# Optimization experiments

Measured on AMD Instinct MI355X. Metric: run time of the kernel, lower is better.

Reference implementation:

```python
import jax, jax.numpy as jnp
import numpy as np

C = 128      # in_channels == global_graph_width
T = 1024     # time_step_len
B = 32       # batch (scenes)
N = B * T    # total nodes
E = 16 * N   # edges


def setup_inputs() -> dict:
    key = jax.random.key(0)
    ks = jax.random.split(key, 10)
    s = 1.0 / np.sqrt(C)
    return {
        "x": jax.random.normal(ks[0], (N, C), dtype=jnp.float32),
        "edge_index": jax.random.randint(ks[1], (2, E), 0, N, dtype=jnp.int64),
        "valid_lens": jax.random.randint(ks[2], (B,), 1, T, dtype=jnp.int64),
        "time_step_len": T,
        "Wq": jax.random.uniform(ks[3], (C, C), jnp.float32, -s, s),
        "bq": jax.random.uniform(ks[4], (C,), jnp.float32, -s, s),
        "Wk": jax.random.uniform(ks[5], (C, C), jnp.float32, -s, s),
        "bk": jax.random.uniform(ks[6], (C,), jnp.float32, -s, s),
        "Wv": jax.random.uniform(ks[7], (C, C), jnp.float32, -s, s),
        "bv": jax.random.uniform(ks[8], (C,), jnp.float32, -s, s),
    }


def reference(x, edge_index, valid_lens, time_step_len, Wq, bq, Wk, bk, Wv, bv):
    # GlobalGraph.forward in eval mode (no random training mask), 1 layer.
    n_nodes, c = x.shape
    xr = x.reshape(-1, time_step_len, c)                    # [B, T, C]
    q = xr @ Wq.T + bq                                      # [B, T, C]
    k = xr @ Wk.T + bk
    v = xr @ Wv.T + bv
    scores = jnp.einsum("btc,bsc->bts", q, k)               # [B, T, T]
    # masked_softmax: each row (b, t) keeps first valid_lens[b] cols, rest -1e6
    col = jnp.arange(time_step_len)                         # [T]
    mask = col[None, None, :] < valid_lens[:, None, None]   # [B, 1, T]
    scores = jnp.where(mask, scores, -1000000.0)
    attn = jax.nn.softmax(scores, axis=-1)                  # [B, T, T]
    out = jnp.einsum("bts,bsc->btc", attn, v).reshape(-1, c)  # [N, C]
    # MessagePassing propagate, aggr='add', flow source_to_target:
    # out_i = sum_{(j->i) in edges} out_j
    src, dst = edge_index[0], edge_index[1]
    return jax.ops.segment_sum(out[src], dst, num_segments=n_nodes)
```

## Files before the change

### kernel.cpp

```cpp
#include <hip/hip_runtime.h>
#include <hip/hip_bf16.h>
#include <stdint.h>

typedef __attribute__((ext_vector_type(8))) short short8;
typedef __attribute__((ext_vector_type(4))) float f32x4;
typedef __attribute__((ext_vector_type(4))) uint32_t u32x4;

static constexpr int NN = 32768;
static constexpr int CC = 128;
static constexpr int TT = 1024;
static constexpr int BB = 32;
static constexpr int EE = 524288;
static constexpr int PAD = 96;
static constexpr unsigned POISON = 0xAAAAAAAAu;

__device__ __forceinline__ unsigned short f2b(float f) {
    uint32_t u = __builtin_bit_cast(uint32_t, f);
    u = (u + 0x7fffu + ((u >> 16) & 1u)) >> 16;
    return (unsigned short)u;
}
__device__ __forceinline__ float b2f(unsigned short u) {
    uint32_t v = ((uint32_t)u) << 16;
    return __builtin_bit_cast(float, v);
}
__device__ __forceinline__ uint32_t cvt_pk_bf16(float lo, float hi) {
    uint32_t r;
    asm("v_cvt_pk_bf16_f32 %0, %1, %2" : "=v"(r) : "v"(lo), "v"(hi));
    return r;
}
__device__ __forceinline__ short8 pack8(float4 f0, float4 f1) {
    u32x4 pk;
    pk[0] = cvt_pk_bf16(f0.x, f0.y); pk[1] = cvt_pk_bf16(f0.z, f0.w);
    pk[2] = cvt_pk_bf16(f1.x, f1.y); pk[3] = cvt_pk_bf16(f1.z, f1.w);
    return __builtin_bit_cast(short8, pk);
}

static constexpr int QP = 132;

__global__ __launch_bounds__(256) void k_qkv(
    const float* __restrict__ Wq, const float* __restrict__ Wk,
    const float* __restrict__ Wv,
    const float* __restrict__ x,
    const float* __restrict__ bq, const float* __restrict__ bk, const float* __restrict__ bv,
    unsigned short* __restrict__ Qb, unsigned short* __restrict__ Kb,
    unsigned short* __restrict__ VB)
{
    __shared__ unsigned short Wl[CC * CC];
    __shared__ unsigned short qsm[4][16 * QP];

    int wv   = threadIdx.x >> 6;
    int lane = threadIdx.x & 63;
    int l15  = lane & 15, quad = lane >> 4;
    int m0   = ((blockIdx.x << 2) + wv) << 4;
    unsigned short* myT = qsm[wv];

    short8 a[4];
    const float* xrow = x + (size_t)(m0 + l15) * CC + quad * 8;
#pragma unroll
    for (int kk = 0; kk < 4; kk++) {
        float4 f0 = *(const float4*)(xrow + kk * 32);
        float4 f1 = *(const float4*)(xrow + kk * 32 + 4);
        a[kk] = pack8(f0, f1);
    }

    int srow = threadIdx.x >> 1;
    int shalf = threadIdx.x & 1;

    const float* Ws[3] = {Wq, Wk, Wv};
    const float* Bs[3] = {bq, bk, bv};

    for (int m = 0; m < 3; m++) {
        __syncthreads();
        {
            const float* wsrc = Ws[m] + (size_t)srow * CC + shalf * 64;
#pragma unroll
            for (int j = 0; j < 8; j++) {
                float4 f0 = *(const float4*)(wsrc + j * 8);
                float4 f1 = *(const float4*)(wsrc + j * 8 + 4);
                short8 v = pack8(f0, f1);
                int byte = srow * 256 + shalf * 128 + j * 16;
                byte ^= (srow & 7) << 4;
                *(short8*)((char*)Wl + byte) = v;
            }
        }
        __syncthreads();

        const float* bias = Bs[m];
        if (m < 2) {
            for (int nt = 0; nt < 8; nt++) {
                int n0 = nt << 4;
                int n  = n0 + l15;
                f32x4 acc = {0.f, 0.f, 0.f, 0.f};
#pragma unroll
                for (int kk = 0; kk < 4; kk++) {
                    int byte = n * 256 + kk * 64 + quad * 16;
                    byte ^= (n & 7) << 4;
                    short8 bfrag = *(const short8*)((const char*)Wl + byte);
                    acc = __builtin_amdgcn_mfma_f32_16x16x32_bf16(a[kk], bfrag, acc, 0, 0, 0);
                }
                float bval = bias[n];
#pragma unroll
                for (int r = 0; r < 4; r++)
                    myT[(quad * 4 + r) * QP + n] = f2b(acc[r] + bval);
            }
            unsigned short* dstp = m ? Kb : Qb;
#pragma unroll
            for (int t = 0; t < 4; t++) {
                int g   = t * 64 + lane;
                int row = g >> 4;
                int gc  = (g & 15) * 8;
                short8 vvx = *(const short8*)&myT[row * QP + gc];
                *(short8*)&dstp[(size_t)(m0 + row) * CC + gc] = vvx;
            }
        } else {
            for (int nt = 0; nt < 8; nt++) {
                int n0 = nt << 4;
                int n  = n0 + l15;
                f32x4 acc = {0.f, 0.f, 0.f, 0.f};
#pragma unroll
                for (int kk = 0; kk < 4; kk++) {
                    int byte = n * 256 + kk * 64 + quad * 16;
                    byte ^= (n & 7) << 4;
                    short8 bfrag = *(const short8*)((const char*)Wl + byte);
                    acc = __builtin_amdgcn_mfma_f32_16x16x32_bf16(a[kk], bfrag, acc, 0, 0, 0);
                }
                float bval = bias[n];
                ushort4 pk;
                pk.x = f2b(acc[0] + bval); pk.y = f2b(acc[1] + bval);
                pk.z = f2b(acc[2] + bval); pk.w = f2b(acc[3] + bval);
                int b_  = m0 >> 10;
                int sb  = (m0 & (TT - 1)) >> 5;
                int sin = (m0 & 31) + quad * 4;
                *(ushort4*)&VB[((size_t)(b_ * 32 + sb) * CC + n) * 32 + sin] = pk;
            }
        }
    }
}

static constexpr int PITCH = 40;

__global__ __launch_bounds__(256, 2) void k_attn(
    const unsigned short* __restrict__ Qb, const unsigned short* __restrict__ Kb,
    const unsigned short* __restrict__ VB, const int* __restrict__ valid_lens,
    unsigned short* __restrict__ ao2,
    const int* __restrict__ ei, int* __restrict__ cnt, int* __restrict__ slot)
{
    __shared__ unsigned short Ksm[3][512 * 8];
    __shared__ unsigned short Vsm[3][512 * 8];
    __shared__ unsigned short pl[4][16 * PITCH];

    int bid  = blockIdx.x;
    int w    = threadIdx.x >> 6;
    int lane = threadIdx.x & 63;
    int l15  = lane & 15, quad = lane >> 4;
    int xcd = bid & 7, j = bid >> 3;
    int b   = xcd + ((j & 3) << 3);
    int qt  = j >> 2;
    int m0  = b * TT + qt * 64 + w * 16;
    int L   = valid_lens[b];
    int nsteps = (L + 31) >> 5;

    int g    = (w << 6) | lane;
    int ksr  = g >> 4,  ksc = ((g & 15) - ksr) & 15;
    int vch  = g >> 2,  vsg = ((g & 3) - (vch >> 1)) & 3;

    const unsigned short* Kbase = Kb + (size_t)b * TT * CC;
    const unsigned short* Vbase = VB + (size_t)b * 32 * CC * 32;

#define STAGE(bufi, s0g)                                                              \
    do {                                                                              \
        int _s0 = (s0g);                                                              \
        __builtin_amdgcn_global_load_lds(                                             \
            (const __attribute__((address_space(1))) uint32_t*)(Kbase + (size_t)(_s0 + ksr) * CC + ksc * 8), \
            (__attribute__((address_space(3))) uint32_t*)&Ksm[bufi][(size_t)(w << 6) * 8], 16, 0, 0);        \
        __builtin_amdgcn_global_load_lds(                                             \
            (const __attribute__((address_space(1))) uint32_t*)(Kbase + (size_t)(_s0 + 16 + ksr) * CC + ksc * 8), \
            (__attribute__((address_space(3))) uint32_t*)&Ksm[bufi][(size_t)((w << 6) + 256) * 8], 16, 0, 0);     \
        const unsigned short* _vt = Vbase + (size_t)(_s0 >> 5) * CC * 32;             \
        __builtin_amdgcn_global_load_lds(                                             \
            (const __attribute__((address_space(1))) uint32_t*)(_vt + vch * 32 + vsg * 8),                   \
            (__attribute__((address_space(3))) uint32_t*)&Vsm[bufi][(size_t)(w << 6) * 8], 16, 0, 0);        \
        __builtin_amdgcn_global_load_lds(                                             \
            (const __attribute__((address_space(1))) uint32_t*)(_vt + (vch + 64) * 32 + vsg * 8),            \
            (__attribute__((address_space(3))) uint32_t*)&Vsm[bufi][(size_t)((w << 6) + 256) * 8], 16, 0, 0);     \
    } while (0)

    short8 a[4];
    {
        const unsigned short* qrow = Qb + (size_t)(m0 + l15) * CC + quad * 8;
#pragma unroll
        for (int kk = 0; kk < 4; kk++) a[kk] = *(const short8*)(qrow + kk * 32);
    }

    f32x4 o[8];
#pragma unroll
    for (int ct = 0; ct < 8; ct++) o[ct] = (f32x4){0.f, 0.f, 0.f, 0.f};
    float l_[4] = {0.f, 0.f, 0.f, 0.f};

    unsigned short* myP = pl[w];

    STAGE(0, 0);
    if (nsteps > 1) STAGE(1, 32);

    for (int i = 0; i < nsteps; i++) {
        int s0 = i << 5;
        int bufi = i - (i / 3) * 3;
        int rem = nsteps - 1 - i;
        if (rem >= 1) asm volatile("s_waitcnt vmcnt(4)" ::: "memory");
        else          asm volatile("s_waitcnt vmcnt(0)" ::: "memory");
        __builtin_amdgcn_s_barrier();
        __builtin_amdgcn_sched_barrier(0);

        const unsigned short* Kc = Ksm[bufi];
        const unsigned short* Vc = Vsm[bufi];

        f32x4 S0 = {0.f,0.f,0.f,0.f}, S1 = {0.f,0.f,0.f,0.f};
        __builtin_amdgcn_s_setprio(1);
#pragma unroll
        for (int kk = 0; kk < 4; kk++) {
            int cidx = kk * 4 + quad;
            int t0 = (cidx + l15) & 15;
            short8 b0 = *(const short8*)&Kc[(size_t)(l15 * 16 + t0) * 8];
            short8 b1 = *(const short8*)&Kc[(size_t)(((16 | l15) * 16) + t0) * 8];
            S0 = __builtin_amdgcn_mfma_f32_16x16x32_bf16(a[kk], b0, S0, 0, 0, 0);
            S1 = __builtin_amdgcn_mfma_f32_16x16x32_bf16(a[kk], b1, S1, 0, 0, 0);
        }
        __builtin_amdgcn_s_setprio(0);

        bool ok0 = (s0 + l15) < L;
        bool ok1 = (s0 + 16 + l15) < L;
        float p0[4], p1[4];
#pragma unroll
        for (int r = 0; r < 4; r++) {
            p0[r] = ok0 ? __expf(S0[r]) : 0.f;
            p1[r] = ok1 ? __expf(S1[r]) : 0.f;
            l_[r] += p0[r] + p1[r];
        }
#pragma unroll
        for (int r = 0; r < 4; r++) {
            int row = quad * 4 + r;
            myP[row * PITCH + l15]      = f2b(p0[r]);
            myP[row * PITCH + 16 + l15] = f2b(p1[r]);
        }
        short8 pf = *(const short8*)(myP + l15 * PITCH + quad * 8);
        __builtin_amdgcn_s_setprio(1);
#pragma unroll
        for (int ct = 0; ct < 8; ct++) {
            int c  = (ct << 4) | l15;
            int sg = (quad + (c >> 1)) & 3;
            short8 vf = *(const short8*)&Vc[(size_t)(c * 4 + sg) * 8];
            o[ct] = __builtin_amdgcn_mfma_f32_16x16x32_bf16(pf, vf, o[ct], 0, 0, 0);
        }
        __builtin_amdgcn_s_setprio(0);

        if (i + 2 < nsteps) {
            int nb = i + 2;
            STAGE(nb - (nb / 3) * 3, nb << 5);
        }
    }

#pragma unroll
    for (int r = 0; r < 4; r++) {
#pragma unroll
        for (int off = 1; off < 16; off <<= 1) l_[r] += __shfl_xor(l_[r], off, 16);
    }

    float rl[4];
#pragma unroll
    for (int r = 0; r < 4; r++) rl[r] = 1.0f / l_[r];
#pragma unroll
    for (int ct = 0; ct < 8; ct++)
#pragma unroll
        for (int r = 0; r < 4; r++)
            ao2[(size_t)(m0 + quad * 4 + r) * CC + ct * 16 + l15] = f2b(o[ct][r] * rl[r]);

    {
        int e0 = (bid << 10) + threadIdx.x;
#pragma unroll
        for (int k2 = 0; k2 < 4; k2++) {
            int e = e0 + (k2 << 8);
            int src = ei[e];
            int dst = ei[EE + e];
            int pos = (int)((unsigned)atomicAdd(&cnt[dst], 1) - POISON);
            if (pos < PAD) slot[(size_t)dst * PAD + pos] = src;
        }
    }
#undef STAGE
}

__global__ __launch_bounds__(256) void k_gather(
    const int* __restrict__ cnt, const int* __restrict__ slot,
    const unsigned short* __restrict__ ao2, float* __restrict__ out)
{
    int node = __builtin_amdgcn_readfirstlane(blockIdx.x * 4 + (threadIdx.x >> 6));
    int lane = threadIdx.x & 63;
    int g    = lane >> 4;
    int l15  = lane & 15;
    int deg  = (int)((unsigned)cnt[node] - POISON);
    deg = min(deg, PAD);
    const int* sl = slot + (size_t)node * PAD;
    const short8* base = (const short8*)ao2;

    float acc[8] = {0.f, 0.f, 0.f, 0.f, 0.f, 0.f, 0.f, 0.f};
    int full = deg >> 2;
    for (int t = 0; t < full; t++) {
        int src = sl[(t << 2) | g];
        short8 v = base[(size_t)src * 16 + l15];
#pragma unroll
        for (int c = 0; c < 8; c++) acc[c] += b2f((unsigned short)v[c]);
    }
    int rem = deg & 3;
    if (rem) {
        bool ok = g < rem;
        int idx = (full << 2) + (ok ? g : 0);
        int src = sl[idx];
        short8 v = base[(size_t)src * 16 + l15];
        if (ok) {
#pragma unroll
            for (int c = 0; c < 8; c++) acc[c] += b2f((unsigned short)v[c]);
        }
    }
#pragma unroll
    for (int c = 0; c < 8; c++) {
        acc[c] += __shfl_xor(acc[c], 16);
        acc[c] += __shfl_xor(acc[c], 32);
    }
    float* orow = out + (size_t)node * CC + l15 * 8;
    if (g == 0) {
        float4 lo; lo.x = acc[0]; lo.y = acc[1]; lo.z = acc[2]; lo.w = acc[3];
        *(float4*)orow = lo;
    } else if (g == 1) {
        float4 hi; hi.x = acc[4]; hi.y = acc[5]; hi.z = acc[6]; hi.w = acc[7];
        *(float4*)(orow + 4) = hi;
    }
}

extern "C" void kernel_launch(void* const* d_in, const int* in_sizes, int n_in,
                              void* d_out, int out_size, void* d_ws, size_t ws_size,
                              hipStream_t stream) {
    const float* x  = (const float*)d_in[0];
    const int*   ei = (const int*)d_in[1];
    const int*   vl = (const int*)d_in[2];
    const float* Wq = (const float*)d_in[4];
    const float* bq = (const float*)d_in[5];
    const float* Wk = (const float*)d_in[6];
    const float* bk = (const float*)d_in[7];
    const float* Wv = (const float*)d_in[8];
    const float* bv = (const float*)d_in[9];

    char* ws = (char*)d_ws;
    unsigned short* Qb   = (unsigned short*)(ws + 8486912);
    unsigned short* Kb   = (unsigned short*)(ws + 16875520);
    unsigned short* VB   = (unsigned short*)(ws + 25264128);
    unsigned short* ao2  = (unsigned short*)(ws + 67469312);
    int*            slot = (int*)(ws + 75857920);
    int*            cnt  = (int*)(ws + 88440832);
    float*          out  = (float*)d_out;

    k_qkv   <<<512,  256, 0, stream>>>(Wq, Wk, Wv, x, bq, bk, bv, Qb, Kb, VB);
    k_attn  <<<512,  256, 0, stream>>>(Qb, Kb, VB, vl, ao2, ei, cnt, slot);
    k_gather<<<NN/4, 256, 0, stream>>>(cnt, slot, ao2, out);
}
```

Measured before the change: 167.6 us.

## Process two 16-row query tiles per wave to reuse K/V fragments

Each wave in the attention kernel now handles 32 query rows instead of 16. It does this with two A-fragment sets and two output accumulators that share the same K and V LDS reads, so the grid is halved and each block does twice the edge-scatter work. The aim is to cut LDS and global K/V traffic per query and amortise staging and barrier overhead. The cost is more live registers and fewer blocks: 256 for 256 CUs, which lowers latency hiding and makes imbalance from varying valid_lens worse.

New measurement: 174.1 us. 1.04x slower.

```diff
diff --git a/kernel.cpp b/kernel.cpp
--- a/kernel.cpp
+++ b/kernel.cpp
@@ -147,7 +147,7 @@
 {
     __shared__ unsigned short Ksm[3][512 * 8];
     __shared__ unsigned short Vsm[3][512 * 8];
-    __shared__ unsigned short pl[4][16 * PITCH];
+    __shared__ unsigned short pl[4][2][16 * PITCH];
 
     int bid  = blockIdx.x;
     int w    = threadIdx.x >> 6;
@@ -156,7 +156,7 @@
     int xcd = bid & 7, j = bid >> 3;
     int b   = xcd + ((j & 3) << 3);
     int qt  = j >> 2;
-    int m0  = b * TT + qt * 64 + w * 16;
+    int m0  = b * TT + qt * 128 + w * 32;
     int L   = valid_lens[b];
     int nsteps = (L + 31) >> 5;
 
@@ -185,19 +185,27 @@
             (__attribute__((address_space(3))) uint32_t*)&Vsm[bufi][(size_t)((w << 6) + 256) * 8], 16, 0, 0);     \
     } while (0)
 
-    short8 a[4];
+    short8 a0[4], a1[4];
     {
         const unsigned short* qrow = Qb + (size_t)(m0 + l15) * CC + quad * 8;
 #pragma unroll
-        for (int kk = 0; kk < 4; kk++) a[kk] = *(const short8*)(qrow + kk * 32);
-    }
-
-    f32x4 o[8];
-#pragma unroll
-    for (int ct = 0; ct < 8; ct++) o[ct] = (f32x4){0.f, 0.f, 0.f, 0.f};
-    float l_[4] = {0.f, 0.f, 0.f, 0.f};
-
-    unsigned short* myP = pl[w];
+        for (int kk = 0; kk < 4; kk++) a0[kk] = *(const short8*)(qrow + kk * 32);
+        qrow += 16 * CC;
+#pragma unroll
+        for (int kk = 0; kk < 4; kk++) a1[kk] = *(const short8*)(qrow + kk * 32);
+    }
+
+    f32x4 oa[8], ob[8];
+#pragma unroll
+    for (int ct = 0; ct < 8; ct++) {
+        oa[ct] = (f32x4){0.f, 0.f, 0.f, 0.f};
+        ob[ct] = (f32x4){0.f, 0.f, 0.f, 0.f};
+    }
+    float la[4] = {0.f, 0.f, 0.f, 0.f};
+    float lb[4] = {0.f, 0.f, 0.f, 0.f};
+
+    unsigned short* myPa = pl[w][0];
+    unsigned short* myPb = pl[w][1];
 
     STAGE(0, 0);
     if (nsteps > 1) STAGE(1, 32);
@@ -214,7 +222,8 @@
         const unsigned short* Kc = Ksm[bufi];
         const unsigned short* Vc = Vsm[bufi];
 
-        f32x4 S0 = {0.f,0.f,0.f,0.f}, S1 = {0.f,0.f,0.f,0.f};
+        f32x4 S0a = {0.f,0.f,0.f,0.f}, S1a = {0.f,0.f,0.f,0.f};
+        f32x4 S0b = {0.f,0.f,0.f,0.f}, S1b = {0.f,0.f,0.f,0.f};
         __builtin_amdgcn_s_setprio(1);
 #pragma unroll
         for (int kk = 0; kk < 4; kk++) {
@@ -222,34 +231,43 @@
             int t0 = (cidx + l15) & 15;
             short8 b0 = *(const short8*)&Kc[(size_t)(l15 * 16 + t0) * 8];
             short8 b1 = *(const short8*)&Kc[(size_t)(((16 | l15) * 16) + t0) * 8];
-            S0 = __builtin_amdgcn_mfma_f32_16x16x32_bf16(a[kk], b0, S0, 0, 0, 0);
-            S1 = __builtin_amdgcn_mfma_f32_16x16x32_bf16(a[kk], b1, S1, 0, 0, 0);
+            S0a = __builtin_amdgcn_mfma_f32_16x16x32_bf16(a0[kk], b0, S0a, 0, 0, 0);
+            S1a = __builtin_amdgcn_mfma_f32_16x16x32_bf16(a0[kk], b1, S1a, 0, 0, 0);
+            S0b = __builtin_amdgcn_mfma_f32_16x16x32_bf16(a1[kk], b0, S0b, 0, 0, 0);
+            S1b = __builtin_amdgcn_mfma_f32_16x16x32_bf16(a1[kk], b1, S1b, 0, 0, 0);
         }
         __builtin_amdgcn_s_setprio(0);
 
         bool ok0 = (s0 + l15) < L;
         bool ok1 = (s0 + 16 + l15) < L;
-        float p0[4], p1[4];
+        float p0a[4], p1a[4], p0b[4], p1b[4];
 #pragma unroll
         for (int r = 0; r < 4; r++) {
-            p0[r] = ok0 ? __expf(S0[r]) : 0.f;
-            p1[r] = ok1 ? __expf(S1[r]) : 0.f;
-            l_[r] += p0[r] + p1[r];
+            p0a[r] = ok0 ? __expf(S0a[r]) : 0.f;
+            p1a[r] = ok1 ? __expf(S1a[r]) : 0.f;
+            p0b[r] = ok0 ? __expf(S0b[r]) : 0.f;
+            p1b[r] = ok1 ? __expf(S1b[r]) : 0.f;
+            la[r] += p0a[r] + p1a[r];
+            lb[r] += p0b[r] + p1b[r];
         }
 #pragma unroll
         for (int r = 0; r < 4; r++) {
             int row = quad * 4 + r;
-            myP[row * PITCH + l15]      = f2b(p0[r]);
-            myP[row * PITCH + 16 + l15] = f2b(p1[r]);
-        }
-        short8 pf = *(const short8*)(myP + l15 * PITCH + quad * 8);
+            myPa[row * PITCH + l15]      = f2b(p0a[r]);
+            myPa[row * PITCH + 16 + l15] = f2b(p1a[r]);
+            myPb[row * PITCH + l15]      = f2b(p0b[r]);
+            myPb[row * PITCH + 16 + l15] = f2b(p1b[r]);
+        }
+        short8 pfa = *(const short8*)(myPa + l15 * PITCH + quad * 8);
+        short8 pfb = *(const short8*)(myPb + l15 * PITCH + quad * 8);
         __builtin_amdgcn_s_setprio(1);
 #pragma unroll
         for (int ct = 0; ct < 8; ct++) {
             int c  = (ct << 4) | l15;
             int sg = (quad + (c >> 1)) & 3;
             short8 vf = *(const short8*)&Vc[(size_t)(c * 4 + sg) * 8];
-            o[ct] = __builtin_amdgcn_mfma_f32_16x16x32_bf16(pf, vf, o[ct], 0, 0, 0);
+            oa[ct] = __builtin_amdgcn_mfma_f32_16x16x32_bf16(pfa, vf, oa[ct], 0, 0, 0);
+            ob[ct] = __builtin_amdgcn_mfma_f32_16x16x32_bf16(pfb, vf, ob[ct], 0, 0, 0);
         }
         __builtin_amdgcn_s_setprio(0);
 
@@ -262,22 +280,27 @@
 #pragma unroll
     for (int r = 0; r < 4; r++) {
 #pragma unroll
-        for (int off = 1; off < 16; off <<= 1) l_[r] += __shfl_xor(l_[r], off, 16);
-    }
-
-    float rl[4];
-#pragma unroll
-    for (int r = 0; r < 4; r++) rl[r] = 1.0f / l_[r];
+        for (int off = 1; off < 16; off <<= 1) {
+            la[r] += __shfl_xor(la[r], off, 16);
+            lb[r] += __shfl_xor(lb[r], off, 16);
+        }
+    }
+
+    float rla[4], rlb[4];
+#pragma unroll
+    for (int r = 0; r < 4; r++) { rla[r] = 1.0f / la[r]; rlb[r] = 1.0f / lb[r]; }
 #pragma unroll
     for (int ct = 0; ct < 8; ct++)
 #pragma unroll
-        for (int r = 0; r < 4; r++)
-            ao2[(size_t)(m0 + quad * 4 + r) * CC + ct * 16 + l15] = f2b(o[ct][r] * rl[r]);
+        for (int r = 0; r < 4; r++) {
+            ao2[(size_t)(m0 + quad * 4 + r) * CC + ct * 16 + l15]      = f2b(oa[ct][r] * rla[r]);
+            ao2[(size_t)(m0 + 16 + quad * 4 + r) * CC + ct * 16 + l15] = f2b(ob[ct][r] * rlb[r]);
+        }
 
     {
-        int e0 = (bid << 10) + threadIdx.x;
-#pragma unroll
-        for (int k2 = 0; k2 < 4; k2++) {
+        int e0 = (bid << 11) + threadIdx.x;
+#pragma unroll
+        for (int k2 = 0; k2 < 8; k2++) {
             int e = e0 + (k2 << 8);
             int src = ei[e];
             int dst = ei[EE + e];
@@ -358,6 +381,6 @@
     float*          out  = (float*)d_out;
 
     k_qkv   <<<512,  256, 0, stream>>>(Wq, Wk, Wv, x, bq, bk, bv, Qb, Kb, VB);
-    k_attn  <<<512,  256, 0, stream>>>(Qb, Kb, VB, vl, ao2, ei, cnt, slot);
+    k_attn  <<<256,  256, 0, stream>>>(Qb, Kb, VB, vl, ao2, ei, cnt, slot);
     k_gather<<<NN/4, 256, 0, stream>>>(cnt, slot, ao2, out);
 }
```
